# Optimization experiments

Measured on AMD Instinct MI355X. Metric: run time of the kernel, lower is better.

The kernel has to match this reference:

```python
import jax, jax.numpy as jnp
import numpy as np
from jax import lax

NPOINT = 1024
RADIUS = 0.3
NSAMPLE = 64


def setup_inputs() -> dict:
    key = jax.random.key(0)
    ks = jax.random.split(key, 8)
    B, N, C = 4, 16384, 3
    xyz = jax.random.normal(ks[0], (B, N, 3), dtype=jnp.float32)
    features = jax.random.normal(ks[1], (B, N, C), dtype=jnp.float32)
    W1 = jax.random.normal(ks[2], (64, 6), dtype=jnp.float32) / np.sqrt(6.0)
    b1 = jnp.zeros((64,), dtype=jnp.float32)
    W2 = jax.random.normal(ks[3], (64, 64), dtype=jnp.float32) / np.sqrt(64.0)
    b2 = jnp.zeros((64,), dtype=jnp.float32)
    W3 = jax.random.normal(ks[4], (128, 64), dtype=jnp.float32) / np.sqrt(64.0)
    b3 = jnp.zeros((128,), dtype=jnp.float32)
    return {"xyz": xyz, "features": features, "W1": W1, "b1": b1,
            "W2": W2, "b2": b2, "W3": W3, "b3": b3}


def _fps_single(xyz, npoint):
    """Furthest point sampling for one cloud (N,3) -> (npoint,) int32 indices.
    Matches CUDA FPS: start at index 0, iteratively pick the point furthest
    from the selected set (min-distance maximization)."""
    N = xyz.shape[0]

    def body(carry, _):
        mindist, last = carry
        d = jnp.sum((xyz - xyz[last]) ** 2, axis=-1)  # (N,)
        mindist = jnp.minimum(mindist, d)
        nxt = jnp.argmax(mindist).astype(jnp.int32)
        return (mindist, nxt), nxt

    init = (jnp.full((N,), 1e10, dtype=xyz.dtype), jnp.int32(0))
    _, rest = lax.scan(body, init, None, length=npoint - 1)
    return jnp.concatenate([jnp.zeros((1,), jnp.int32), rest])


def _ball_query(xyz, new_xyz, radius, nsample):
    """xyz (B,N,3), new_xyz (B,P,3) -> (B,P,nsample) int32 indices.
    Matches CUDA ball_query: first nsample points within radius (in index
    order), remaining slots padded with the first valid index."""
    N = xyz.shape[1]
    d2 = jnp.sum((new_xyz[:, :, None, :] - xyz[:, None, :, :]) ** 2, axis=-1)  # (B,P,N)
    inball = d2 < radius * radius
    order = jnp.where(inball, jnp.arange(N, dtype=jnp.int32), jnp.int32(N))
    # k smallest indices == top_k of negated order
    idx = -lax.top_k(-order, nsample)[0]  # (B,P,nsample), sorted ascending
    first = idx[..., :1]
    idx = jnp.where(idx < N, idx, first)   # pad with first valid index
    idx = jnp.where(idx < N, idx, 0)       # safety if no neighbor at all
    return idx


def reference(xyz, features, W1, b1, W2, b2, W3, b3):
    B, N, _ = xyz.shape
    # --- FPS + gather centers ---
    fps_idx = jax.vmap(lambda p: _fps_single(p, NPOINT))(xyz)       # (B,P)
    bidx = jnp.arange(B)[:, None]
    new_xyz = xyz[bidx, fps_idx]                                    # (B,P,3)
    # --- ball query + grouping (QueryAndGroup with use_xyz=True) ---
    idx = _ball_query(xyz, new_xyz, RADIUS, NSAMPLE)                # (B,P,S)
    bidx2 = jnp.arange(B)[:, None, None]
    grouped_xyz = xyz[bidx2, idx] - new_xyz[:, :, None, :]          # (B,P,S,3)
    grouped_feat = features[bidx2, idx]                             # (B,P,S,C)
    g = jnp.concatenate([grouped_xyz, grouped_feat], axis=-1)       # (B,P,S,3+C)
    g = jnp.transpose(g, (0, 3, 1, 2))                              # (B,Cin,P,S)
    # --- shared MLP: 1x1 conv2d + ReLU stack ---
    h = jax.nn.relu(jnp.einsum('oc,bcps->bops', W1, g) + b1[None, :, None, None])
    h = jax.nn.relu(jnp.einsum('oc,bcps->bops', W2, h) + b2[None, :, None, None])
    h = jax.nn.relu(jnp.einsum('oc,bcps->bops', W3, h) + b3[None, :, None, None])
    # --- max-pool over the neighbor (sample) dim ---
    new_features = jnp.max(h, axis=-1)                              # (B,128,P)
    return new_xyz, new_features
```

## Files before the change

kernel.cpp:

```cpp
#include <hip/hip_runtime.h>

#define N_PTS   16384
#define NPOINT  1024
#define NSAMPLE 64
#define R2 ((float)(0.3 * 0.3))

__global__ __launch_bounds__(1024, 1) void fps_kernel(
    const float* __restrict__ xyz, float* __restrict__ out_newxyz) {
    const int b = blockIdx.x;
    const int t = threadIdx.x;
    const float* __restrict__ X = xyz + (size_t)b * N_PTS * 3;

    float px[16], py[16], pz[16], md[16];
#pragma unroll
    for (int j = 0; j < 16; ++j) {
        int n = j * 1024 + t;
        px[j] = X[3 * n];
        py[j] = X[3 * n + 1];
        pz[j] = X[3 * n + 2];
        md[j] = 1e10f;
    }

    __shared__ __align__(16) float s_val[16];
    __shared__ int s_win[2];
    if (t == 0) { s_win[0] = 0x7fffffff; s_win[1] = 0x7fffffff; }

    float lx = X[0], ly = X[1], lz = X[2];
    if (t == 0) {
        out_newxyz[b * NPOINT * 3 + 0] = lx;
        out_newxyz[b * NPOINT * 3 + 1] = ly;
        out_newxyz[b * NPOINT * 3 + 2] = lz;
    }
    __syncthreads();

    for (int i = 1; i < NPOINT; ++i) {
        float tv = -1.0f;
#pragma unroll
        for (int j = 0; j < 16; ++j) {
            float dx = px[j] - lx, dy = py[j] - ly, dz = pz[j] - lz;
            float d = dx * dx + dy * dy + dz * dz;
            float m = fminf(md[j], d);
            md[j] = m;
            tv = fmaxf(tv, m);
        }
        float wv = tv;
#pragma unroll
        for (int off = 32; off > 0; off >>= 1)
            wv = fmaxf(wv, __shfl_xor(wv, off, 64));
        if ((t & 63) == 0) s_val[t >> 6] = wv;
        __syncthreads();
        const float4* sv4 = reinterpret_cast<const float4*>(s_val);
        float4 a0 = sv4[0], a1 = sv4[1], a2 = sv4[2], a3 = sv4[3];
        float f0 = fmaxf(fmaxf(a0.x, a0.y), fmaxf(a0.z, a0.w));
        float f1 = fmaxf(fmaxf(a1.x, a1.y), fmaxf(a1.z, a1.w));
        float f2 = fmaxf(fmaxf(a2.x, a2.y), fmaxf(a2.z, a2.w));
        float f3 = fmaxf(fmaxf(a3.x, a3.y), fmaxf(a3.z, a3.w));
        float fv = fmaxf(fmaxf(f0, f1), fmaxf(f2, f3));
        if (tv == fv) {
            int cand = 0x7fffffff;
#pragma unroll
            for (int j = 15; j >= 0; --j)
                cand = (md[j] == fv) ? (j * 1024 + t) : cand;
            atomicMin(&s_win[i & 1], cand);
        }
        __syncthreads();
        int fi = s_win[i & 1];
        if (t == 0) s_win[(i & 1) ^ 1] = 0x7fffffff;
        int fis = __builtin_amdgcn_readfirstlane(fi);
        const float* __restrict__ Xw = X + 3 * fis;
        lx = Xw[0]; ly = Xw[1]; lz = Xw[2];
        if (t == 0) {
            float* o = out_newxyz + b * NPOINT * 3 + 3 * i;
            o[0] = lx; o[1] = ly; o[2] = lz;
        }
    }
}

__global__ __launch_bounds__(256, 2) void bq_mlp_kernel(
    const float* __restrict__ xyz, const float* __restrict__ feat,
    const float* __restrict__ W1, const float* __restrict__ b1,
    const float* __restrict__ W2, const float* __restrict__ b2,
    const float* __restrict__ W3, const float* __restrict__ b3,
    const float* __restrict__ newxyz, float* __restrict__ out) {
    const int wave = threadIdx.x >> 6;
    const int lane = threadIdx.x & 63;
    const int q = blockIdx.x * 4 + wave;
    const int b = q >> 10;
    const int p = q & 1023;
    const float* __restrict__ X = xyz  + (size_t)b * N_PTS * 3;
    const float* __restrict__ F = feat + (size_t)b * N_PTS * 3;

    const float cx = newxyz[3 * q], cy = newxyz[3 * q + 1], cz = newxyz[3 * q + 2];

    __shared__ __align__(16) float g[4][NSAMPLE][8];
    __shared__ __align__(16) float h[4][NSAMPLE][64];

    float w1r[6];
#pragma unroll
    for (int k = 0; k < 6; ++k) w1r[k] = W1[lane * 6 + k];
    const float b1r = b1[lane];
    const float b2r = b2[lane];

    int count = 0;
    for (int base = 0; base < N_PTS; base += 64) {
        int n = base + lane;
        float x = X[3 * n], y = X[3 * n + 1], z = X[3 * n + 2];
        float dx = x - cx, dy = y - cy, dz = z - cz;
        float d2 = dx * dx + dy * dy + dz * dz;
        bool in = d2 < R2;
        unsigned long long mask = __ballot(in);
        int slot = count + __popcll(mask & ((1ull << lane) - 1ull));
        if (in && slot < NSAMPLE) {
            g[wave][slot][0] = dx; g[wave][slot][1] = dy; g[wave][slot][2] = dz;
            g[wave][slot][3] = F[3 * n]; g[wave][slot][4] = F[3 * n + 1];
            g[wave][slot][5] = F[3 * n + 2];
        }
        count += __popcll(mask);
        if (count >= NSAMPLE) break;
    }
    asm volatile("s_waitcnt lgkmcnt(0)" ::: "memory");
    if (count == 0) {
        float x = X[0], y = X[1], z = X[2];
        g[wave][lane][0] = x - cx; g[wave][lane][1] = y - cy; g[wave][lane][2] = z - cz;
        g[wave][lane][3] = F[0];   g[wave][lane][4] = F[1];   g[wave][lane][5] = F[2];
    } else if (lane >= count) {
        float v0 = g[wave][0][0], v1 = g[wave][0][1], v2 = g[wave][0][2];
        float v3 = g[wave][0][3], v4 = g[wave][0][4], v5 = g[wave][0][5];
        g[wave][lane][0] = v0; g[wave][lane][1] = v1; g[wave][lane][2] = v2;
        g[wave][lane][3] = v3; g[wave][lane][4] = v4; g[wave][lane][5] = v5;
    }
    __syncthreads();

    for (int s = 0; s < NSAMPLE; ++s) {
        const float4* g4 = reinterpret_cast<const float4*>(&g[wave][s][0]);
        float4 ga = g4[0], gb = g4[1];
        float a = fmaf(w1r[0], ga.x, b1r);
        a = fmaf(w1r[1], ga.y, a);
        a = fmaf(w1r[2], ga.z, a);
        a = fmaf(w1r[3], ga.w, a);
        a = fmaf(w1r[4], gb.x, a);
        a = fmaf(w1r[5], gb.y, a);
        h[wave][s][lane] = fmaxf(a, 0.0f);
    }
    __syncthreads();

    float w2r[64];
    {
        const float4* w4 = reinterpret_cast<const float4*>(W2 + (size_t)lane * 64);
#pragma unroll
        for (int cc = 0; cc < 16; ++cc) *reinterpret_cast<float4*>(&w2r[4 * cc]) = w4[cc];
    }

#pragma unroll 2
    for (int s = 0; s < NSAMPLE; ++s) {
        float a0 = 0.f, a1 = 0.f, a2 = 0.f, a3 = 0.f;
        const float4* h4 = reinterpret_cast<const float4*>(&h[wave][s][0]);
#pragma unroll
        for (int cc = 0; cc < 16; ++cc) {
            float4 hv = h4[cc];
            a0 = fmaf(w2r[4 * cc + 0], hv.x, a0);
            a1 = fmaf(w2r[4 * cc + 1], hv.y, a1);
            a2 = fmaf(w2r[4 * cc + 2], hv.z, a2);
            a3 = fmaf(w2r[4 * cc + 3], hv.w, a3);
        }
        float v = fmaxf(b2r + ((a0 + a1) + (a2 + a3)), 0.0f);
        h[wave][s][lane] = v;
    }
    __syncthreads();

    float w3a[64], w3b[64];
    {
        const float4* wa = reinterpret_cast<const float4*>(W3 + (size_t)lane * 64);
        const float4* wb = reinterpret_cast<const float4*>(W3 + (size_t)(lane + 64) * 64);
#pragma unroll
        for (int cc = 0; cc < 16; ++cc) {
            *reinterpret_cast<float4*>(&w3a[4 * cc]) = wa[cc];
            *reinterpret_cast<float4*>(&w3b[4 * cc]) = wb[cc];
        }
    }
    const float b3r0 = b3[lane];
    const float b3r1 = b3[lane + 64];

    float m0 = 0.0f, m1 = 0.0f;
#pragma unroll 2
    for (int s = 0; s < NSAMPLE; ++s) {
        float a0 = 0.f, a1 = 0.f, a2 = 0.f, a3 = 0.f;
        float c0 = 0.f, c1 = 0.f, c2 = 0.f, c3 = 0.f;
        const float4* h4 = reinterpret_cast<const float4*>(&h[wave][s][0]);
#pragma unroll
        for (int cc = 0; cc < 16; ++cc) {
            float4 hv = h4[cc];
            a0 = fmaf(w3a[4 * cc + 0], hv.x, a0);
            a1 = fmaf(w3a[4 * cc + 1], hv.y, a1);
            a2 = fmaf(w3a[4 * cc + 2], hv.z, a2);
            a3 = fmaf(w3a[4 * cc + 3], hv.w, a3);
            c0 = fmaf(w3b[4 * cc + 0], hv.x, c0);
            c1 = fmaf(w3b[4 * cc + 1], hv.y, c1);
            c2 = fmaf(w3b[4 * cc + 2], hv.z, c2);
            c3 = fmaf(w3b[4 * cc + 3], hv.w, c3);
        }
        float v0 = fmaxf(b3r0 + ((a0 + a1) + (a2 + a3)), 0.0f);
        float v1 = fmaxf(b3r1 + ((c0 + c1) + (c2 + c3)), 0.0f);
        m0 = fmaxf(m0, v0);
        m1 = fmaxf(m1, v1);
    }
    out[(size_t)b * 128 * NPOINT + (size_t)lane        * NPOINT + p] = m0;
    out[(size_t)b * 128 * NPOINT + (size_t)(lane + 64) * NPOINT + p] = m1;
}

extern "C" void kernel_launch(void* const* d_in, const int* in_sizes, int n_in,
                              void* d_out, int out_size, void* d_ws, size_t ws_size,
                              hipStream_t stream) {
    const float* xyz  = (const float*)d_in[0];
    const float* feat = (const float*)d_in[1];
    const float* W1   = (const float*)d_in[2];
    const float* b1   = (const float*)d_in[3];
    const float* W2   = (const float*)d_in[4];
    const float* b2   = (const float*)d_in[5];
    const float* W3   = (const float*)d_in[6];
    const float* b3   = (const float*)d_in[7];
    float* out = (float*)d_out;

    float* out_newxyz = out;
    float* out_feat   = out + 4 * NPOINT * 3;

    fps_kernel<<<4, 1024, 0, stream>>>(xyz, out_newxyz);
    bq_mlp_kernel<<<1024, 256, 0, stream>>>(xyz, feat, W1, b1, W2, b2, W3, b3,
                                            out_newxyz, out_feat);
}
```

Baseline: 2.082 ms.

## Restructure FPS to 512 threads with packed math and single-barrier reduction

The furthest-point-sampling kernel now uses 512 threads per block, each holding 32 points in float2 vector registers so the distance math can use packed FP32 ops. The per-iteration argmax now takes one barrier instead of two. Each wave's winning lane writes its max value and that point's coordinates to shared memory, and every thread picks the block winner from those entries, which removes the atomicMin and the dependent global reload of the chosen point. Tie-breaking now follows wave order with strict greater-than instead of a global minimum index, which should match because waves cover interleaved ranges. Register pressure doubles per thread, and ties between waves may pick a different index than before.

```diff
diff --git a/kernel.cpp b/kernel.cpp
--- a/kernel.cpp
+++ b/kernel.cpp
@@ -5,25 +5,33 @@
 #define NSAMPLE 64
 #define R2 ((float)(0.3 * 0.3))
 
-__global__ __launch_bounds__(1024, 1) void fps_kernel(
+typedef float v2f __attribute__((ext_vector_type(2)));
+
+#define FPS_T  512
+#define PPT    (N_PTS / FPS_T)
+#define NPAIR  (PPT / 2)
+#define NWAVE  (FPS_T / 64)
+
+__global__ __launch_bounds__(FPS_T, 2) void fps_kernel(
     const float* __restrict__ xyz, float* __restrict__ out_newxyz) {
     const int b = blockIdx.x;
     const int t = threadIdx.x;
+    const int wave = t >> 6;
+    const int lane = t & 63;
     const float* __restrict__ X = xyz + (size_t)b * N_PTS * 3;
 
-    float px[16], py[16], pz[16], md[16];
-#pragma unroll
-    for (int j = 0; j < 16; ++j) {
-        int n = j * 1024 + t;
-        px[j] = X[3 * n];
-        py[j] = X[3 * n + 1];
-        pz[j] = X[3 * n + 2];
-        md[j] = 1e10f;
-    }
-
-    __shared__ __align__(16) float s_val[16];
-    __shared__ int s_win[2];
-    if (t == 0) { s_win[0] = 0x7fffffff; s_win[1] = 0x7fffffff; }
+    v2f px[NPAIR], py[NPAIR], pz[NPAIR], md[NPAIR];
+#pragma unroll
+    for (int j = 0; j < NPAIR; ++j) {
+        int nA = (2 * j) * FPS_T + t;
+        int nB = (2 * j + 1) * FPS_T + t;
+        px[j].x = X[3 * nA];     px[j].y = X[3 * nB];
+        py[j].x = X[3 * nA + 1]; py[j].y = X[3 * nB + 1];
+        pz[j].x = X[3 * nA + 2]; pz[j].y = X[3 * nB + 2];
+        md[j].x = 1e10f;         md[j].y = 1e10f;
+    }
+
+    __shared__ __align__(16) float4 s_best[2][NWAVE];
 
     float lx = X[0], ly = X[1], lz = X[2];
     if (t == 0) {
@@ -31,44 +39,48 @@
         out_newxyz[b * NPOINT * 3 + 1] = ly;
         out_newxyz[b * NPOINT * 3 + 2] = lz;
     }
-    __syncthreads();
 
     for (int i = 1; i < NPOINT; ++i) {
-        float tv = -1.0f;
-#pragma unroll
-        for (int j = 0; j < 16; ++j) {
-            float dx = px[j] - lx, dy = py[j] - ly, dz = pz[j] - lz;
-            float d = dx * dx + dy * dy + dz * dz;
-            float m = fminf(md[j], d);
+        v2f lx2, ly2, lz2;
+        lx2.x = lx; lx2.y = lx;
+        ly2.x = ly; ly2.y = ly;
+        lz2.x = lz; lz2.y = lz;
+        v2f tv2;
+        tv2.x = -1.0f; tv2.y = -1.0f;
+#pragma unroll
+        for (int j = 0; j < NPAIR; ++j) {
+            v2f dx = px[j] - lx2, dy = py[j] - ly2, dz = pz[j] - lz2;
+            v2f d = dx * dx + dy * dy + dz * dz;
+            v2f m;
+            m.x = fminf(md[j].x, d.x);
+            m.y = fminf(md[j].y, d.y);
             md[j] = m;
-            tv = fmaxf(tv, m);
-        }
+            tv2.x = fmaxf(tv2.x, m.x);
+            tv2.y = fmaxf(tv2.y, m.y);
+        }
+        float tv = fmaxf(tv2.x, tv2.y);
         float wv = tv;
 #pragma unroll
         for (int off = 32; off > 0; off >>= 1)
             wv = fmaxf(wv, __shfl_xor(wv, off, 64));
-        if ((t & 63) == 0) s_val[t >> 6] = wv;
+        unsigned long long mask = __ballot(tv == wv);
+        if (lane == (int)__builtin_ctzll(mask)) {
+            float bx = 0.f, by = 0.f, bz = 0.f;
+#pragma unroll
+            for (int j = NPAIR - 1; j >= 0; --j) {
+                if (md[j].y == wv) { bx = px[j].y; by = py[j].y; bz = pz[j].y; }
+                if (md[j].x == wv) { bx = px[j].x; by = py[j].x; bz = pz[j].x; }
+            }
+            s_best[i & 1][wave] = make_float4(wv, bx, by, bz);
+        }
         __syncthreads();
-        const float4* sv4 = reinterpret_cast<const float4*>(s_val);
-        float4 a0 = sv4[0], a1 = sv4[1], a2 = sv4[2], a3 = sv4[3];
-        float f0 = fmaxf(fmaxf(a0.x, a0.y), fmaxf(a0.z, a0.w));
-        float f1 = fmaxf(fmaxf(a1.x, a1.y), fmaxf(a1.z, a1.w));
-        float f2 = fmaxf(fmaxf(a2.x, a2.y), fmaxf(a2.z, a2.w));
-        float f3 = fmaxf(fmaxf(a3.x, a3.y), fmaxf(a3.z, a3.w));
-        float fv = fmaxf(fmaxf(f0, f1), fmaxf(f2, f3));
-        if (tv == fv) {
-            int cand = 0x7fffffff;
-#pragma unroll
-            for (int j = 15; j >= 0; --j)
-                cand = (md[j] == fv) ? (j * 1024 + t) : cand;
-            atomicMin(&s_win[i & 1], cand);
-        }
-        __syncthreads();
-        int fi = s_win[i & 1];
-        if (t == 0) s_win[(i & 1) ^ 1] = 0x7fffffff;
-        int fis = __builtin_amdgcn_readfirstlane(fi);
-        const float* __restrict__ Xw = X + 3 * fis;
-        lx = Xw[0]; ly = Xw[1]; lz = Xw[2];
+        float4 best = s_best[i & 1][0];
+#pragma unroll
+        for (int k = 1; k < NWAVE; ++k) {
+            float4 c = s_best[i & 1][k];
+            if (c.x > best.x) best = c;
+        }
+        lx = best.y; ly = best.z; lz = best.w;
         if (t == 0) {
             float* o = out_newxyz + b * NPOINT * 3 + 3 * i;
             o[0] = lx; o[1] = ly; o[2] = lz;
@@ -224,7 +236,7 @@
     float* out_newxyz = out;
     float* out_feat   = out + 4 * NPOINT * 3;
 
-    fps_kernel<<<4, 1024, 0, stream>>>(xyz, out_newxyz);
+    fps_kernel<<<4, FPS_T, 0, stream>>>(xyz, out_newxyz);
     bq_mlp_kernel<<<1024, 256, 0, stream>>>(xyz, feat, W1, b1, W2, b2, W3, b3,
                                             out_newxyz, out_feat);
 }
```

After: 2.683 ms. +28.9%, slower.
